# Kernel tuning notes

Hardware: AMD Instinct MI355X
Metric: run time of the kernel (lower is better)

The kernel has to match this reference:

```python
import jax, jax.numpy as jnp
import numpy as np

D_MODEL = 1024
N_HEADS = 16
D_KEYS = 64
D_LLM = 4096
Q_RANK = 512
KV_RANK = 512
EPS = 1e-5


def layernorm(x, g, b):
    mu = jnp.mean(x, axis=-1, keepdims=True)
    var = jnp.mean(jnp.square(x - mu), axis=-1, keepdims=True)
    return (x - mu) * jax.lax.rsqrt(var + EPS) * g + b


def setup_inputs() -> dict:
    key = jax.random.key(0)
    ks = jax.random.split(key, 10)
    te = jax.random.normal(ks[0], (4, 1024, D_MODEL), jnp.float32)
    se = jax.random.normal(ks[1], (1000, D_LLM), jnp.float32)
    s = 0.02
    return {
        'target_embedding': te,
        'source_embedding': se,
        'value_embedding': se,  # module asserts source == value
        'q_a_w': jax.random.normal(ks[2], (Q_RANK, D_MODEL), jnp.float32) * s,
        'q_ln_g': jnp.ones((Q_RANK,), jnp.float32),
        'q_ln_b': jnp.zeros((Q_RANK,), jnp.float32),
        'q_b_w': jax.random.normal(ks[3], (N_HEADS * D_KEYS, Q_RANK), jnp.float32) * s,
        'kv_a_w': jax.random.normal(ks[4], (KV_RANK, D_LLM), jnp.float32) * s,
        'kv_ln_g': jnp.ones((KV_RANK,), jnp.float32),
        'kv_ln_b': jnp.zeros((KV_RANK,), jnp.float32),
        'kv_b_w': jax.random.normal(ks[5], (N_HEADS * 2 * D_KEYS, KV_RANK), jnp.float32) * s,
        'out_w': jax.random.normal(ks[6], (D_LLM, N_HEADS * D_KEYS), jnp.float32) * s,
        'out_b': jnp.zeros((D_LLM,), jnp.float32),
    }


def reference(target_embedding, source_embedding, value_embedding,
              q_a_w, q_ln_g, q_ln_b, q_b_w,
              kv_a_w, kv_ln_g, kv_ln_b, kv_b_w, out_w, out_b):
    B, L, _ = target_embedding.shape
    S = source_embedding.shape[0]
    # Q path: LoRA down -> LN -> up, [B,L,H,E]
    q = layernorm(target_embedding @ q_a_w.T, q_ln_g, q_ln_b) @ q_b_w.T
    q = q.reshape(B, L, N_HEADS, D_KEYS)
    # KV path (no batch dim, broadcast across B)
    ckv = layernorm(source_embedding @ kv_a_w.T, kv_ln_g, kv_ln_b)  # [S, r]
    kv = (ckv @ kv_b_w.T).reshape(S, N_HEADS, 2 * D_KEYS)
    k, v = kv[..., :D_KEYS], kv[..., D_KEYS:]  # [S,H,E] each
    scale = 1.0 / np.sqrt(D_KEYS)
    scores = jnp.einsum('blhe,she->bhls', q, k)  # [B,H,L,S]
    A = jax.nn.softmax(scale * scores, axis=-1)  # dropout inactive (eval)
    out = jnp.einsum('bhls,she->blhe', A, v).reshape(B, L, N_HEADS * D_KEYS)
    return out @ out_w.T + out_b
```

## Files before the change

kernel.cpp:

```cpp
#include <hip/hip_runtime.h>

typedef unsigned short u16;
typedef __bf16 bf16x8 __attribute__((ext_vector_type(8)));
typedef float f32x4 __attribute__((ext_vector_type(4)));

#define DEV __device__ __forceinline__

DEV u16 f2bf(float f){
  unsigned u = __float_as_uint(f);
  u += 0x7fff + ((u >> 16) & 1);
  return (u16)(u >> 16);
}
DEV float bf2f(u16 v){ return __uint_as_float(((unsigned)v) << 16); }

DEV void gll16(const void* g, void* l){
  __builtin_amdgcn_global_load_lds(
    (__attribute__((address_space(1))) unsigned int*)(unsigned long long)g,
    (__attribute__((address_space(3))) unsigned int*)(unsigned int)(unsigned long long)l,
    16, 0, 0);
}

template<int WM, int WN, int OBF, int BIAS>
__global__ __launch_bounds__(256) void gemm_bt(
    const u16* __restrict__ A, int lda, long sA1, long sA2,
    const u16* __restrict__ B, int ldb, long sB1, long sB2,
    void* __restrict__ Cv, int ldc, long sC1, long sC2,
    const float* __restrict__ bias,
    int M, int N, int K, int Z2)
{
  constexpr int BM = WM*64, BN = WN*64;
  constexpr int NW = WM*WN;
  constexpr int A_INSTS = BM/16, B_INSTS = BN/16;
  constexpr int APW = A_INSTS/NW, BPW = B_INSTS/NW;
  __shared__ u16 sA[BM*32];
  __shared__ u16 sB[BN*32];
  const int tid  = threadIdx.x;
  const int wave = tid >> 6, lane = tid & 63;
  const int quad = lane >> 4, l16 = lane & 15;
  const int wm = wave % WM, wn = wave / WM;
  const long bm = blockIdx.y, bn = blockIdx.x;
  const int z  = blockIdx.z;
  const int z1 = z / Z2, z2 = z - z1*Z2;
  const u16* Ab = A + z1*sA1 + z2*sA2 + bm*BM*(long)lda;
  const u16* Bb = B + z1*sB1 + z2*sB2 + bn*BN*(long)ldb;

  f32x4 acc[4][4] = {};

  for (int k0 = 0; k0 < K; k0 += 32){
    __syncthreads();
#pragma unroll
    for (int j = 0; j < APW; j++){
      const int inst = wave*APW + j;
      const int o = inst*1024 + lane*16;
      const int row = o >> 6, colb = o & 63;
      gll16(Ab + (long)row*lda + k0 + (colb >> 1), &sA[inst*512]);
    }
#pragma unroll
    for (int j = 0; j < BPW; j++){
      const int inst = wave*BPW + j;
      const int o = inst*1024 + lane*16;
      const int row = o >> 6, colb = o & 63;
      gll16(Bb + (long)row*ldb + k0 + (colb >> 1), &sB[inst*512]);
    }
    __syncthreads();
    bf16x8 af[4], bfr[4];
#pragma unroll
    for (int mi = 0; mi < 4; mi++)
      af[mi] = *(const bf16x8*)&sA[(wm*64 + mi*16 + l16)*32 + quad*8];
#pragma unroll
    for (int ni = 0; ni < 4; ni++)
      bfr[ni] = *(const bf16x8*)&sB[(wn*64 + ni*16 + l16)*32 + quad*8];
#pragma unroll
    for (int mi = 0; mi < 4; mi++)
#pragma unroll
      for (int ni = 0; ni < 4; ni++)
        acc[mi][ni] = __builtin_amdgcn_mfma_f32_16x16x32_bf16(af[mi], bfr[ni], acc[mi][ni], 0, 0, 0);
  }

  const long crow0 = bm*BM + wm*64 + quad*4;
  const long ccol0 = bn*BN + wn*64 + l16;
  if (OBF){
    u16* Cp = (u16*)Cv + z1*sC1 + z2*sC2;
#pragma unroll
    for (int mi = 0; mi < 4; mi++)
#pragma unroll
      for (int ni = 0; ni < 4; ni++)
#pragma unroll
        for (int r = 0; r < 4; r++)
          Cp[(crow0 + mi*16 + r)*ldc + ccol0 + ni*16] = f2bf(acc[mi][ni][r]);
  } else {
    float* Cp = (float*)Cv + z1*sC1 + z2*sC2;
    float bv[4] = {0.f,0.f,0.f,0.f};
    if (BIAS){
#pragma unroll
      for (int ni = 0; ni < 4; ni++) bv[ni] = bias[ccol0 + ni*16];
    }
#pragma unroll
    for (int mi = 0; mi < 4; mi++)
#pragma unroll
      for (int ni = 0; ni < 4; ni++)
#pragma unroll
        for (int r = 0; r < 4; r++)
          Cp[(crow0 + mi*16 + r)*ldc + ccol0 + ni*16] = acc[mi][ni][r] + bv[ni];
  }
}

__global__ __launch_bounds__(256) void cvt_all(
    const float* __restrict__ te,   const float* __restrict__ qaw,
    const float* __restrict__ qbw,  const float* __restrict__ kvaw,
    const float* __restrict__ kvbw, const float* __restrict__ outw,
    const float* __restrict__ se,
    u16* __restrict__ te_bf, u16* __restrict__ qa_bf, u16* __restrict__ qb_bf,
    u16* __restrict__ kva_bf, u16* __restrict__ kvb_bf,
    u16* __restrict__ outw_bf, u16* __restrict__ se_bf)
{
  const long NG = 4194304;
  for (long g = (long)blockIdx.x*256 + threadIdx.x; g < NG; g += (long)gridDim.x*256){
    const float* src; u16* dst; long rel; bool zero = false;
    if (g < 1048576)      { src=te;   dst=te_bf;   rel=g; }
    else if (g < 1179648) { src=qaw;  dst=qa_bf;   rel=g-1048576; }
    else if (g < 1310720) { src=qbw;  dst=qb_bf;   rel=g-1179648; }
    else if (g < 1835008) { src=kvaw; dst=kva_bf;  rel=g-1310720; }
    else if (g < 2097152) { src=kvbw; dst=kvb_bf;  rel=g-1835008; }
    else if (g < 3145728) { src=outw; dst=outw_bf; rel=g-2097152; }
    else                  { src=se;   dst=se_bf;   rel=g-3145728; zero = (rel>>10) >= 1000; }
    ushort4 o;
    if (!zero){
      float4 v = *(const float4*)(src + rel*4);
      o.x = f2bf(v.x); o.y = f2bf(v.y); o.z = f2bf(v.z); o.w = f2bf(v.w);
    } else { o.x = 0; o.y = 0; o.z = 0; o.w = 0; }
    *(ushort4*)(dst + rel*4) = o;
  }
}

__global__ __launch_bounds__(256) void ln_both(
    u16* __restrict__ out_q,  const float* __restrict__ in_q,
    const float* __restrict__ qg, const float* __restrict__ qb_,
    u16* __restrict__ out_kv, const float* __restrict__ in_kv,
    const float* __restrict__ kg, const float* __restrict__ kb_)
{
  long row; const float* in; u16* outp; const float* gam; const float* bet;
  int nparts; long pstride; int valid;
  if (blockIdx.x < 4096){
    row = blockIdx.x; in = in_q; outp = out_q; gam = qg; bet = qb_;
    nparts = 2; pstride = 4096L*512; valid = 1;
  } else {
    row = blockIdx.x - 4096; in = in_kv; outp = out_kv; gam = kg; bet = kb_;
    nparts = 8; pstride = 1024L*512; valid = (row < 1000);
  }
  const int tid = threadIdx.x;
  u16* op = outp + row*512 + tid*2;
  if (!valid){
    ushort2 z; z.x = 0; z.y = 0;
    *(ushort2*)op = z;
    return;
  }
  float2 x; x.x = 0.f; x.y = 0.f;
  for (int p = 0; p < nparts; p++){
    float2 v = *(const float2*)(in + p*pstride + row*512 + tid*2);
    x.x += v.x; x.y += v.y;
  }
  float s  = x.x + x.y;
  float s2 = x.x*x.x + x.y*x.y;
#pragma unroll
  for (int m = 32; m; m >>= 1){ s += __shfl_xor(s, m, 64); s2 += __shfl_xor(s2, m, 64); }
  __shared__ float red[8];
  const int wave = tid >> 6, lane = tid & 63;
  if (lane == 0){ red[wave*2] = s; red[wave*2+1] = s2; }
  __syncthreads();
  float ts = red[0]+red[2]+red[4]+red[6];
  float t2 = red[1]+red[3]+red[5]+red[7];
  float mu  = ts * (1.f/512.f);
  float var = t2 * (1.f/512.f) - mu*mu;
  float rs  = rsqrtf(var + 1e-5f);
  float2 g2 = *(const float2*)(gam + tid*2);
  float2 b2 = *(const float2*)(bet + tid*2);
  ushort2 o;
  o.x = f2bf((x.x - mu)*rs*g2.x + b2.x);
  o.y = f2bf((x.y - mu)*rs*g2.y + b2.y);
  *(ushort2*)op = o;
}

__global__ __launch_bounds__(256) void split_kv(
    const float* __restrict__ kv, u16* __restrict__ kbf, u16* __restrict__ vT)
{
  const int h  = blockIdx.x;
  const int sc = blockIdx.y;
  const int s0 = sc*64;
  const long PST = 1024L*2048;
  __shared__ u16 tile[64][65];
  const int e  = threadIdx.x & 63;
  const int sg = threadIdx.x >> 6;
#pragma unroll
  for (int i = 0; i < 16; i++){
    const int sl = i*4 + sg;
    const int s = s0 + sl;
    float kvl = kv[(long)s*2048 + h*128 + e]      + kv[PST + (long)s*2048 + h*128 + e];
    float vvl = kv[(long)s*2048 + h*128 + 64 + e] + kv[PST + (long)s*2048 + h*128 + 64 + e];
    kbf[((long)h*1024 + s)*64 + ((e + 8*s) & 63)] = f2bf(kvl);
    tile[sl][e] = f2bf(vvl);
  }
  __syncthreads();
#pragma unroll
  for (int i = 0; i < 16; i++){
    const int er = i*4 + sg;
    const int s  = s0 + e;
    const int t128 = s >> 7, pos = s & 127;
    vT[(((long)h*8 + t128)*64 + er)*128 + ((pos + 8*er) & 127)] = tile[e][er];
  }
}

__global__ __launch_bounds__(256) void flash_attn(
    const u16* __restrict__ Q, const u16* __restrict__ Kt,
    const u16* __restrict__ Vt, u16* __restrict__ O)
{
  __shared__ u16 sKV[128*64];
  __shared__ u16 sPT[128*136];
  __shared__ __align__(16) float sAl[128];
  const int tid = threadIdx.x, w = tid >> 6, lane = tid & 63;
  const int quad = lane >> 4, l16 = lane & 15;
  const int h = blockIdx.y;
  const long q0 = (long)blockIdx.x * 128;

  bf16x8 bq[2][2];
#pragma unroll
  for (int ni = 0; ni < 2; ni++)
#pragma unroll
    for (int kf = 0; kf < 2; kf++)
      bq[ni][kf] = *(const bf16x8*)&Q[(q0 + w*32 + ni*16 + l16)*1024 + h*64 + kf*32 + quad*8];

  f32x4 accO[2][4] = {};
  float mst[2] = {-3e38f, -3e38f};
  float lst[2] = {0.f, 0.f};

  for (int it = 0; it < 8; it++){
    const int s0 = it*128;
    __syncthreads();
#pragma unroll
    for (int j = 0; j < 4; j++){
      const int inst = w*4 + j;
      gll16(Kt + (long)h*65536 + (long)s0*64 + inst*512 + lane*8, &sKV[inst*512]);
    }
    __syncthreads();

    f32x4 accS[8][2] = {};
#pragma unroll
    for (int kf = 0; kf < 2; kf++)
#pragma unroll
      for (int mi = 0; mi < 8; mi++){
        const int sr = mi*16 + l16;
        bf16x8 ka = *(const bf16x8*)&sKV[sr*64 + ((kf*32 + quad*8 + 8*sr) & 63)];
#pragma unroll
        for (int ni = 0; ni < 2; ni++)
          accS[mi][ni] = __builtin_amdgcn_mfma_f32_16x16x32_bf16(ka, bq[ni][kf], accS[mi][ni], 0, 0, 0);
      }

#pragma unroll
    for (int ni = 0; ni < 2; ni++){
      float tm = -3e38f;
#pragma unroll
      for (int mi = 0; mi < 8; mi++)
#pragma unroll
        for (int r = 0; r < 4; r++){
          float v = accS[mi][ni][r] * 0.125f;
          const int s = s0 + mi*16 + quad*4 + r;
          v = (s < 1000) ? v : -3e38f;
          accS[mi][ni][r] = v;
          tm = fmaxf(tm, v);
        }
      tm = fmaxf(tm, __shfl_xor(tm, 16, 64));
      tm = fmaxf(tm, __shfl_xor(tm, 32, 64));
      const float mnew = fmaxf(mst[ni], tm);
      const float al = __expf(mst[ni] - mnew);
      mst[ni] = mnew;
      float sum = 0.f;
      const int qloc = w*32 + ni*16 + l16;
#pragma unroll
      for (int mi = 0; mi < 8; mi++){
        float p0 = __expf(accS[mi][ni][0] - mnew);
        float p1 = __expf(accS[mi][ni][1] - mnew);
        float p2 = __expf(accS[mi][ni][2] - mnew);
        float p3 = __expf(accS[mi][ni][3] - mnew);
        sum += (p0 + p1) + (p2 + p3);
        ushort4 pk;
        pk.x = f2bf(p0); pk.y = f2bf(p1); pk.z = f2bf(p2); pk.w = f2bf(p3);
        *(ushort4*)&sPT[qloc*136 + mi*16 + quad*4] = pk;
      }
      sum += __shfl_xor(sum, 16, 64);
      sum += __shfl_xor(sum, 32, 64);
      lst[ni] = lst[ni]*al + sum;
      if (quad == 0) sAl[qloc] = al;
    }
    __syncthreads();
#pragma unroll
    for (int j = 0; j < 4; j++){
      const int inst = w*4 + j;
      gll16(Vt + ((long)(h*8 + it))*8192 + inst*512 + lane*8, &sKV[inst*512]);
    }
#pragma unroll
    for (int mi = 0; mi < 2; mi++){
      f32x4 al4 = *(const f32x4*)&sAl[w*32 + mi*16 + quad*4];
#pragma unroll
      for (int ni = 0; ni < 4; ni++)
        accO[mi][ni] *= al4;
    }
    __syncthreads();

#pragma unroll
    for (int kf = 0; kf < 4; kf++){
      bf16x8 pa[2], vb[4];
#pragma unroll
      for (int mi = 0; mi < 2; mi++)
        pa[mi] = *(const bf16x8*)&sPT[(w*32 + mi*16 + l16)*136 + kf*32 + quad*8];
#pragma unroll
      for (int ni = 0; ni < 4; ni++){
        const int e = ni*16 + l16;
        vb[ni] = *(const bf16x8*)&sKV[e*128 + ((kf*32 + quad*8 + 8*e) & 127)];
      }
#pragma unroll
      for (int mi = 0; mi < 2; mi++)
#pragma unroll
        for (int ni = 0; ni < 4; ni++)
          accO[mi][ni] = __builtin_amdgcn_mfma_f32_16x16x32_bf16(pa[mi], vb[ni], accO[mi][ni], 0, 0, 0);
    }
  }

  __syncthreads();
  if (quad == 0){ sAl[w*32 + l16] = lst[0]; sAl[w*32 + 16 + l16] = lst[1]; }
  __syncthreads();
#pragma unroll
  for (int mi = 0; mi < 2; mi++){
    f32x4 l4 = *(const f32x4*)&sAl[w*32 + mi*16 + quad*4];
#pragma unroll
    for (int ni = 0; ni < 4; ni++)
#pragma unroll
      for (int r = 0; r < 4; r++)
        O[(q0 + w*32 + mi*16 + quad*4 + r)*1024 + h*64 + ni*16 + l16] =
            f2bf(accO[mi][ni][r] / l4[r]);
  }
}

extern "C" void kernel_launch(void* const* d_in, const int* in_sizes, int n_in,
                              void* d_out, int out_size, void* d_ws, size_t ws_size,
                              hipStream_t stream)
{
  const float* te   = (const float*)d_in[0];
  const float* se   = (const float*)d_in[1];
  const float* qaw  = (const float*)d_in[3];
  const float* qlg  = (const float*)d_in[4];
  const float* qlb  = (const float*)d_in[5];
  const float* qbw  = (const float*)d_in[6];
  const float* kvaw = (const float*)d_in[7];
  const float* kvlg = (const float*)d_in[8];
  const float* kvlb = (const float*)d_in[9];
  const float* kvbw = (const float*)d_in[10];
  const float* outw = (const float*)d_in[11];
  const float* outb = (const float*)d_in[12];
  float* out = (float*)d_out;
  (void)ws_size; (void)in_sizes; (void)n_in; (void)out_size;

  char* ws = (char*)d_ws;
  const size_t MB = 1024*1024;
  u16*   te_bf  = (u16*)  (ws + 0*MB);
  u16*   se_bf  = (u16*)  (ws + 8*MB);
  float* qlat   = (float*)(ws + 16*MB);
  float* ckvp   = (float*)(ws + 32*MB);
  float* kvf    = (float*)(ws + 48*MB);
  u16*   qa_bf   = (u16*)(ws + 64*MB);
  u16*   qb_bf   = (u16*)(ws + 65*MB);
  u16*   kva_bf  = (u16*)(ws + 66*MB);
  u16*   kvb_bf  = (u16*)(ws + 70*MB);
  u16*   outw_bf = (u16*)(ws + 72*MB);
  u16*   qln_bf  = (u16*)(ws + 80*MB);
  u16*   q_bf    = (u16*)(ws + 84*MB);
  u16*   ckv_bf  = (u16*)(ws + 92*MB);
  u16*   k_bf    = (u16*)(ws + 93*MB);
  u16*   vT_bf   = (u16*)(ws + 95*MB);
  u16*   attn_bf = (u16*)(ws + 97*MB);

  cvt_all<<<4096, 256, 0, stream>>>(
      te, qaw, qbw, kvaw, kvbw, outw, se,
      te_bf, qa_bf, qb_bf, kva_bf, kvb_bf, outw_bf, se_bf);

  gemm_bt<2,2,0,0><<<dim3(4, 32, 2), 256, 0, stream>>>(
      te_bf, 1024, 512, 0, qa_bf, 1024, 512, 0,
      qlat, 512, 4096L*512, 0, nullptr, 4096, 512, 512, 1);
  gemm_bt<2,2,0,0><<<dim3(4, 8, 8), 256, 0, stream>>>(
      se_bf, 4096, 512, 0, kva_bf, 4096, 512, 0,
      ckvp, 512, 1024L*512, 0, nullptr, 1024, 512, 512, 1);
  ln_both<<<4096 + 1024, 256, 0, stream>>>(
      qln_bf, qlat, qlg, qlb, ckv_bf, ckvp, kvlg, kvlb);
  gemm_bt<2,2,1,0><<<dim3(8, 32, 1), 256, 0, stream>>>(
      qln_bf, 512, 0,0, qb_bf, 512, 0,0, q_bf, 1024, 0,0, nullptr, 4096, 1024, 512, 1);
  gemm_bt<2,2,0,0><<<dim3(16, 8, 2), 256, 0, stream>>>(
      ckv_bf, 512, 256, 0, kvb_bf, 512, 256, 0,
      kvf, 2048, 1024L*2048, 0, nullptr, 1024, 2048, 256, 1);
  split_kv<<<dim3(16, 16), 256, 0, stream>>>(kvf, k_bf, vT_bf);

  flash_attn<<<dim3(32, 16), 256, 0, stream>>>(q_bf, k_bf, vT_bf, attn_bf);

  gemm_bt<2,2,0,1><<<dim3(32, 32, 1), 256, 0, stream>>>(
      attn_bf, 1024, 0,0, outw_bf, 1024, 0,0, out, 4096, 0,0, outb, 4096, 4096, 1024, 1);
}
```

Baseline: 323.8 us.

## Use 256x256-tile double-buffered MFMA GEMM with XCD swizzle for output projection

Adds a new GEMM kernel for the final output projection (4096x4096x1024). It uses 512-thread blocks and 256x256 output tiles with double-buffered LDS staging through global_load_lds, an XOR-swizzled LDS layout, a ping-pong four-phase MFMA schedule with setprio, and a block-id remap that spreads tiles across XCDs. The larger tile is meant to raise arithmetic intensity and cut global traffic compared with the 128x128 generic kernel. In exchange it uses 128KB of LDS per block and fewer blocks (256), which limits occupancy.

```diff
diff --git a/kernel.cpp b/kernel.cpp
--- a/kernel.cpp
+++ b/kernel.cpp
@@ -103,6 +103,173 @@
         for (int r = 0; r < 4; r++)
           Cp[(crow0 + mi*16 + r)*ldc + ccol0 + ni*16] = acc[mi][ni][r] + bv[ni];
   }
+}
+
+__global__ __launch_bounds__(512, 2) void gemm256(
+    const u16* __restrict__ A, const u16* __restrict__ B,
+    float* __restrict__ C, const float* __restrict__ bias,
+    int N, int K, int TN)
+{
+  __shared__ __align__(16) u16 sA[32768];
+  __shared__ __align__(16) u16 sB[32768];
+  const int tid  = threadIdx.x;
+  const int w    = tid >> 6, lane = tid & 63;
+  const int quad = lane >> 4, l16 = lane & 15;
+  const int wm = w >> 2, wn = w & 3;
+  const int cpx = gridDim.x >> 3;
+  const int bid = blockIdx.x;
+  const int wg  = (bid & 7)*cpx + (bid >> 3);
+  const long bm = wg / TN, bn = wg % TN;
+  const int NT = K >> 6;
+
+  const int rsub = lane >> 3;
+  const int kk16 = (lane & 7) ^ rsub;
+  const u16* Ag = A + (bm*256 + w*8 + rsub)*(long)K + kk16*8;
+  const u16* Bg = B + (bn*256 + w*8 + rsub)*(long)K + kk16*8;
+  u16* dA = sA + w*512;
+  u16* dB = sB + w*512;
+
+  auto stage = [&](const u16* G, u16* D, int T){
+#pragma unroll
+    for (int c = 0; c < 4; c++)
+      gll16(G + ((long)c*64)*K + T*64, D + c*4096);
+  };
+
+  const int xr  = l16 & 7;
+  const int ko0 = ((0*4 + quad) ^ xr) * 8;
+  const int ko1 = ((1*4 + quad) ^ xr) * 8;
+  const u16* rA0 = sA + (wm*128 + l16)*64;
+  const u16* rB0 = sB + (wn*64  + l16)*64;
+
+  f32x4 acc[8][4] = {};
+  bf16x8 aF[4][2];
+
+  stage(Ag, dA, 0);
+  stage(Bg, dB, 0);
+  asm volatile("s_waitcnt vmcnt(0)" ::: "memory");
+  __builtin_amdgcn_s_barrier();
+
+  for (int T = 0; T < NT; ++T){
+    const int buf = T & 1;
+    const u16* rA = rA0 + buf*16384;
+    const u16* rB = rB0 + buf*16384;
+
+    {
+#pragma unroll
+      for (int mi = 0; mi < 4; mi++){
+        aF[mi][0] = *(const bf16x8*)(rA + mi*1024 + ko0);
+        aF[mi][1] = *(const bf16x8*)(rA + mi*1024 + ko1);
+      }
+      bf16x8 bF[2][2];
+#pragma unroll
+      for (int ni = 0; ni < 2; ni++){
+        bF[ni][0] = *(const bf16x8*)(rB + ni*1024 + ko0);
+        bF[ni][1] = *(const bf16x8*)(rB + ni*1024 + ko1);
+      }
+      if (T+1 < NT){
+        stage(Ag, dA + (buf^1)*16384, T+1);
+        stage(Bg, dB + (buf^1)*16384, T+1);
+      }
+      __builtin_amdgcn_s_barrier();
+      asm volatile("s_waitcnt lgkmcnt(0)" ::: "memory");
+      __builtin_amdgcn_sched_barrier(0);
+      __builtin_amdgcn_s_setprio(1);
+#pragma unroll
+      for (int kk = 0; kk < 2; kk++)
+#pragma unroll
+        for (int mi = 0; mi < 4; mi++)
+#pragma unroll
+          for (int ni = 0; ni < 2; ni++)
+            acc[mi][ni] = __builtin_amdgcn_mfma_f32_16x16x32_bf16(aF[mi][kk], bF[ni][kk], acc[mi][ni], 0,0,0);
+      __builtin_amdgcn_s_setprio(0);
+      __builtin_amdgcn_s_barrier();
+    }
+
+    {
+      bf16x8 bF[2][2];
+#pragma unroll
+      for (int ni = 0; ni < 2; ni++){
+        bF[ni][0] = *(const bf16x8*)(rB + (2+ni)*1024 + ko0);
+        bF[ni][1] = *(const bf16x8*)(rB + (2+ni)*1024 + ko1);
+      }
+      __builtin_amdgcn_s_barrier();
+      asm volatile("s_waitcnt lgkmcnt(0)" ::: "memory");
+      __builtin_amdgcn_sched_barrier(0);
+      __builtin_amdgcn_s_setprio(1);
+#pragma unroll
+      for (int kk = 0; kk < 2; kk++)
+#pragma unroll
+        for (int mi = 0; mi < 4; mi++)
+#pragma unroll
+          for (int ni = 0; ni < 2; ni++)
+            acc[mi][2+ni] = __builtin_amdgcn_mfma_f32_16x16x32_bf16(aF[mi][kk], bF[ni][kk], acc[mi][2+ni], 0,0,0);
+      __builtin_amdgcn_s_setprio(0);
+      __builtin_amdgcn_s_barrier();
+    }
+
+    {
+#pragma unroll
+      for (int mi = 0; mi < 4; mi++){
+        aF[mi][0] = *(const bf16x8*)(rA + (4+mi)*1024 + ko0);
+        aF[mi][1] = *(const bf16x8*)(rA + (4+mi)*1024 + ko1);
+      }
+      bf16x8 bF[2][2];
+#pragma unroll
+      for (int ni = 0; ni < 2; ni++){
+        bF[ni][0] = *(const bf16x8*)(rB + ni*1024 + ko0);
+        bF[ni][1] = *(const bf16x8*)(rB + ni*1024 + ko1);
+      }
+      __builtin_amdgcn_s_barrier();
+      asm volatile("s_waitcnt lgkmcnt(0)" ::: "memory");
+      __builtin_amdgcn_sched_barrier(0);
+      __builtin_amdgcn_s_setprio(1);
+#pragma unroll
+      for (int kk = 0; kk < 2; kk++)
+#pragma unroll
+        for (int mi = 0; mi < 4; mi++)
+#pragma unroll
+          for (int ni = 0; ni < 2; ni++)
+            acc[4+mi][ni] = __builtin_amdgcn_mfma_f32_16x16x32_bf16(aF[mi][kk], bF[ni][kk], acc[4+mi][ni], 0,0,0);
+      __builtin_amdgcn_s_setprio(0);
+      __builtin_amdgcn_s_barrier();
+    }
+
+    {
+      bf16x8 bF[2][2];
+#pragma unroll
+      for (int ni = 0; ni < 2; ni++){
+        bF[ni][0] = *(const bf16x8*)(rB + (2+ni)*1024 + ko0);
+        bF[ni][1] = *(const bf16x8*)(rB + (2+ni)*1024 + ko1);
+      }
+      __builtin_amdgcn_s_barrier();
+      asm volatile("s_waitcnt lgkmcnt(0)" ::: "memory");
+      __builtin_amdgcn_sched_barrier(0);
+      __builtin_amdgcn_s_setprio(1);
+#pragma unroll
+      for (int kk = 0; kk < 2; kk++)
+#pragma unroll
+        for (int mi = 0; mi < 4; mi++)
+#pragma unroll
+          for (int ni = 0; ni < 2; ni++)
+            acc[4+mi][2+ni] = __builtin_amdgcn_mfma_f32_16x16x32_bf16(aF[mi][kk], bF[ni][kk], acc[4+mi][2+ni], 0,0,0);
+      __builtin_amdgcn_s_setprio(0);
+      asm volatile("s_waitcnt vmcnt(0)" ::: "memory");
+      __builtin_amdgcn_s_barrier();
+    }
+  }
+
+  const long crow0 = bm*256 + wm*128 + quad*4;
+  const long ccol0 = bn*256 + wn*64  + l16;
+  float bv[4];
+#pragma unroll
+  for (int ni = 0; ni < 4; ni++) bv[ni] = bias ? bias[ccol0 + ni*16] : 0.f;
+#pragma unroll
+  for (int mi = 0; mi < 8; mi++)
+#pragma unroll
+    for (int ni = 0; ni < 4; ni++)
+#pragma unroll
+      for (int r = 0; r < 4; r++)
+        C[(crow0 + mi*16 + r)*(long)N + ccol0 + ni*16] = acc[mi][ni][r] + bv[ni];
 }
 
 __global__ __launch_bounds__(256) void cvt_all(
@@ -399,6 +566,6 @@
 
   flash_attn<<<dim3(32, 16), 256, 0, stream>>>(q_bf, k_bf, vT_bf, attn_bf);
 
-  gemm_bt<2,2,0,1><<<dim3(32, 32, 1), 256, 0, stream>>>(
-      attn_bf, 1024, 0,0, outw_bf, 1024, 0,0, out, 4096, 0,0, outb, 4096, 4096, 1024, 1);
-}
+  gemm256<<<dim3(256), 512, 0, stream>>>(
+      attn_bf, outw_bf, out, outb, 4096, 1024, 16);
+}
```

After: 307.6 us. 1.05x faster.
